# Performance work log

Hardware: AMD Instinct MI355X
Metric: run time of the kernel (lower is better)

Reference implementation:

```python
import jax, jax.numpy as jnp
import numpy as np

N_NODES = 100000
N_EDGES = 1600000
IN_DIM, HID_DIM, OUT_DIM = 128, 256, 128


def setup_inputs() -> dict:
    key = jax.random.key(0)
    ks = jax.random.split(key, 5)
    x = jax.random.normal(ks[0], (N_NODES, IN_DIM), dtype=jnp.float32)
    src = jax.random.randint(ks[1], (N_EDGES,), 0, N_NODES, dtype=jnp.int64)
    dst = jax.random.randint(ks[2], (N_EDGES,), 0, N_NODES, dtype=jnp.int64)
    # Glorot-ish init for linear weights (DGL GraphConv default), zero bias
    W1 = jax.random.normal(ks[3], (IN_DIM, HID_DIM), dtype=jnp.float32) * (1.0 / np.sqrt(IN_DIM))
    W2 = jax.random.normal(ks[4], (HID_DIM, OUT_DIM), dtype=jnp.float32) * (1.0 / np.sqrt(HID_DIM))
    b1 = jnp.zeros((HID_DIM,), dtype=jnp.float32)
    b2 = jnp.zeros((OUT_DIM,), dtype=jnp.float32)
    return {"x": x, "src": src, "dst": dst, "W1": W1, "b1": b1, "W2": W2, "b2": b2}


def _degree_norms(src, dst, n_nodes):
    # norm='both': D_out(src)^{-1/2} on messages, D_in(dst)^{-1/2} on aggregate;
    # degrees clamped to min 1 as in DGL.
    ones = jnp.ones(src.shape[0], dtype=jnp.float32)
    deg_out = jax.ops.segment_sum(ones, src, num_segments=n_nodes)
    deg_in = jax.ops.segment_sum(ones, dst, num_segments=n_nodes)
    norm_src = jax.lax.rsqrt(jnp.maximum(deg_out, 1.0))
    norm_dst = jax.lax.rsqrt(jnp.maximum(deg_in, 1.0))
    return norm_src, norm_dst


def _graph_conv(x, src, dst, W, b, norm_src, norm_dst):
    h = x * norm_src[:, None]                                  # [N, d]
    agg = jax.ops.segment_sum(h[src], dst, num_segments=x.shape[0])  # [N, d]
    agg = agg * norm_dst[:, None]
    return agg @ W + b


def reference(x, src, dst, W1, b1, W2, b2):
    norm_src, norm_dst = _degree_norms(src, dst, x.shape[0])
    h = jax.nn.relu(_graph_conv(x, src, dst, W1, b1, norm_src, norm_dst))
    out = _graph_conv(h, src, dst, W2, b2, norm_src, norm_dst)
    return out
```

## Files before the change

kernel.cpp:

```cpp
#include <hip/hip_runtime.h>

constexpr int N_NODES = 100000;
constexpr int N_EDGES = 1600000;
constexpr int DIN = 128, DHID = 256, DOUT = 128;

constexpr int NB = 256;
constexpr int BR = 391;
constexpr int CAP = 8192;
constexpr int NBLK1 = 512;
constexpr int CHUNK = (N_EDGES + NBLK1 - 1) / NBLK1;

typedef __bf16 bf16x8 __attribute__((ext_vector_type(8)));
typedef float f32x4 __attribute__((ext_vector_type(4)));

static __device__ __forceinline__ ushort f2bf(float f) {
    uint u = __float_as_uint(f);
    uint r = (u + 0x7FFFu + ((u >> 16) & 1u)) >> 16;
    return (ushort)r;
}
static __device__ __forceinline__ float bf2f(ushort h) {
    return __uint_as_float(((uint)h) << 16);
}
static __device__ __forceinline__ float bflo(uint w) { return __uint_as_float(w << 16); }
static __device__ __forceinline__ float bfhi(uint w) { return __uint_as_float(w & 0xFFFF0000u); }

__global__ __launch_bounds__(256) void part_kernel(const int* __restrict__ src,
                                                   const int* __restrict__ dst,
                                                   int* __restrict__ curA, int* __restrict__ curB,
                                                   uint2* __restrict__ ppair,
                                                   int* __restrict__ psv, int e) {
    __shared__ int hA[NB], hB[NB], rA[NB], rB[NB], cA[NB], cB[NB];
    const int t = threadIdx.x;
    const int b0 = blockIdx.x * CHUNK;
    const int cnt = min(e - b0, CHUNK);
    hA[t] = 0; hB[t] = 0; cA[t] = 0; cB[t] = 0;
    __syncthreads();
    for (int i = t; i < cnt; i += 256) {
        int s = src[b0 + i], d = dst[b0 + i];
        atomicAdd(&hA[d / BR], 1);
        atomicAdd(&hB[s / BR], 1);
    }
    __syncthreads();
    rA[t] = atomicAdd(&curA[t], hA[t]);
    rB[t] = atomicAdd(&curB[t], hB[t]);
    __syncthreads();
    for (int i = t; i < cnt; i += 256) {
        int s = src[b0 + i], d = dst[b0 + i];
        int bd = d / BR;
        int bs = s / BR;
        int p = rA[bd] + atomicAdd(&cA[bd], 1);
        if (p < CAP) ppair[(size_t)bd * CAP + p] = make_uint2((uint)d, (uint)s);
        int q = rB[bs] + atomicAdd(&cB[bs], 1);
        if (q < CAP) psv[(size_t)bs * CAP + q] = s;
    }
}

__global__ __launch_bounds__(512) void csrn_kernel(const int* __restrict__ curA,
                                                   const int* __restrict__ curB,
                                                   const uint2* __restrict__ ppair,
                                                   const int* __restrict__ psv,
                                                   int* __restrict__ csr,
                                                   int* __restrict__ rowstart,
                                                   float* __restrict__ ndst,
                                                   float* __restrict__ nsrc, int n, int e) {
    __shared__ ushort dloc[CAP];
    __shared__ uint sloc[CAP];
    __shared__ int hist[512], sc[512], exc[512], cur[512];
    __shared__ int sbst;
    const int t = threadIdx.x;
    const int b = blockIdx.x;
    const int first = b * BR;
    const int nr = min(BR, n - first);
    const int cntA = min(curA[b], CAP);
    const size_t base = (size_t)b * CAP;

    if (t < 256) sc[t] = curA[t];
    __syncthreads();
    for (int off = 1; off < 256; off <<= 1) {
        int add = 0;
        if (t < 256 && t >= off) add = sc[t - off];
        __syncthreads();
        if (t < 256) sc[t] += add;
        __syncthreads();
    }
    if (t == 0) {
        sbst = (b == 0) ? 0 : sc[b - 1];
        if (b == 0) rowstart[n] = e;
    }
    hist[t] = 0;
    cur[t] = 0;
    __syncthreads();
    const int bst = sbst;

    for (int i = t; i < cntA; i += 512) {
        uint2 ed = ppair[base + i];
        int dl = (int)ed.x - first;
        dloc[i] = (ushort)dl;
        sloc[i] = ed.y;
        atomicAdd(&hist[dl], 1);
    }
    __syncthreads();
    int h = hist[t];
    sc[t] = h;
    __syncthreads();
    for (int off = 1; off < 512; off <<= 1) {
        int add = (t >= off) ? sc[t - off] : 0;
        __syncthreads();
        sc[t] += add;
        __syncthreads();
    }
    exc[t] = sc[t] - h;
    if (t < nr) {
        rowstart[first + t] = bst + exc[t];
        ndst[first + t] = rsqrtf(fmaxf((float)h, 1.0f));
    }
    __syncthreads();
    for (int i = t; i < cntA; i += 512) {
        int dl = dloc[i];
        int p = exc[dl] + atomicAdd(&cur[dl], 1);
        csr[bst + p] = (int)sloc[i];
    }

    __syncthreads();
    hist[t] = 0;
    __syncthreads();
    const int cntB = min(curB[b], CAP);
    for (int i = t; i < cntB; i += 512) atomicAdd(&hist[psv[base + i] - first], 1);
    __syncthreads();
    if (t < nr) nsrc[first + t] = rsqrtf(fmaxf((float)hist[t], 1.0f));
}

__global__ __launch_bounds__(256) void prep_kernel(const float* __restrict__ x,
                                                   const float* __restrict__ nsrc,
                                                   ushort* __restrict__ xb,
                                                   const float* __restrict__ W1,
                                                   ushort* __restrict__ Wt1,
                                                   const float* __restrict__ W2,
                                                   ushort* __restrict__ Wt2, int n) {
    const int nxb = (n * 32 + 255) / 256;
    int blk = blockIdx.x;
    if (blk < nxb) {
        int i = blk * 256 + threadIdx.x;
        if (i < n * 32) {
            int row = i >> 5;
            float s = nsrc[row];
            float4 v = *(const float4*)&x[(size_t)i * 4];
            ushort4 o = {f2bf(v.x * s), f2bf(v.y * s), f2bf(v.z * s), f2bf(v.w * s)};
            *(ushort4*)&xb[(size_t)i * 4] = o;
        }
    } else if (blk < nxb + DIN * DHID / 256) {
        int i = (blk - nxb) * 256 + threadIdx.x;
        int k = i / DHID, c = i - k * DHID;
        Wt1[(size_t)c * DIN + k] = f2bf(W1[i]);
    } else {
        int i = (blk - nxb - DIN * DHID / 256) * 256 + threadIdx.x;
        int k = i / DOUT, c = i - k * DOUT;
        Wt2[(size_t)c * DHID + k] = f2bf(W2[i]);
    }
}

template <bool OUTBF16, bool ADDBIAS>
__global__ __launch_bounds__(256) void aggb_kernel(const ushort* __restrict__ Xb,
                                                   const int* __restrict__ csr,
                                                   const int* __restrict__ rowstart,
                                                   const float* __restrict__ ndst,
                                                   const float* __restrict__ bias,
                                                   float* __restrict__ outf,
                                                   ushort* __restrict__ outb, int n) {
    int g = threadIdx.x >> 4;
    int lane = threadIdx.x & 15;
    int d = blockIdx.x * 16 + g;
    if (d >= n) return;
    int beg = rowstart[d], end = rowstart[d + 1];
    const int fo = lane * 8;
    const ushort* Xp = Xb + fo;
    float acc[8];
#pragma unroll
    for (int j = 0; j < 8; j++) acc[j] = 0.f;

#define ACC8(v)                                 \
    do {                                        \
        acc[0] += bflo(v.x); acc[1] += bfhi(v.x); \
        acc[2] += bflo(v.y); acc[3] += bfhi(v.y); \
        acc[4] += bflo(v.z); acc[5] += bfhi(v.z); \
        acc[6] += bflo(v.w); acc[7] += bfhi(v.w); \
    } while (0)

    int k = beg;
    for (; k + 4 <= end; k += 4) {
        int s0 = csr[k], s1 = csr[k + 1], s2 = csr[k + 2], s3 = csr[k + 3];
        uint4 v0 = *(const uint4*)(Xp + (size_t)s0 * 128);
        uint4 v1 = *(const uint4*)(Xp + (size_t)s1 * 128);
        uint4 v2 = *(const uint4*)(Xp + (size_t)s2 * 128);
        uint4 v3 = *(const uint4*)(Xp + (size_t)s3 * 128);
        ACC8(v0);
        ACC8(v1);
        ACC8(v2);
        ACC8(v3);
    }
    for (; k < end; ++k) {
        uint4 v = *(const uint4*)(Xp + (size_t)csr[k] * 128);
        ACC8(v);
    }
#undef ACC8

    float nd = ndst[d];
#pragma unroll
    for (int j = 0; j < 8; j++) acc[j] *= nd;
    if constexpr (ADDBIAS) {
        float4 b0 = *(const float4*)&bias[fo];
        float4 b1 = *(const float4*)&bias[fo + 4];
        acc[0] += b0.x; acc[1] += b0.y; acc[2] += b0.z; acc[3] += b0.w;
        acc[4] += b1.x; acc[5] += b1.y; acc[6] += b1.z; acc[7] += b1.w;
    }
    if constexpr (OUTBF16) {
        uint4 o;
        o.x = (uint)f2bf(acc[0]) | ((uint)f2bf(acc[1]) << 16);
        o.y = (uint)f2bf(acc[2]) | ((uint)f2bf(acc[3]) << 16);
        o.z = (uint)f2bf(acc[4]) | ((uint)f2bf(acc[5]) << 16);
        o.w = (uint)f2bf(acc[6]) | ((uint)f2bf(acc[7]) << 16);
        *(uint4*)(outb + (size_t)d * 128 + fo) = o;
    } else {
        float4 o0 = {acc[0], acc[1], acc[2], acc[3]};
        float4 o1 = {acc[4], acc[5], acc[6], acc[7]};
        *(float4*)(outf + (size_t)d * 128 + fo) = o0;
        *(float4*)(outf + (size_t)d * 128 + fo + 4) = o1;
    }
}

__global__ __launch_bounds__(256) void fused64_kernel(const ushort* __restrict__ A,
                                                      const ushort* __restrict__ Wt1,
                                                      const float* __restrict__ b1,
                                                      const float* __restrict__ nsrc,
                                                      const ushort* __restrict__ Wt2,
                                                      ushort* __restrict__ T, int M) {
    __shared__ ushort Sa[64][128];
    __shared__ ushort H1[64][128];
    const int row0 = blockIdx.x * 64;
    const int t = threadIdx.x;
    const int w = t >> 6, lane = t & 63;
    const int l16 = lane & 15, lk = lane >> 4;

#pragma unroll
    for (int i = 0; i < 4; i++) {
        int idx = i * 256 + t;
        int r = idx >> 4, oct = idx & 15;
        int gr = row0 + r;
        uint4 v = make_uint4(0u, 0u, 0u, 0u);
        if (gr < M) v = *(const uint4*)&A[(size_t)gr * 128 + oct * 8];
        *(uint4*)((char*)&Sa[0][0] + r * 256 + (oct ^ (r & 15)) * 16) = v;
    }
    __syncthreads();

    f32x4 acc2[4][2];
#pragma unroll
    for (int i = 0; i < 4; i++)
#pragma unroll
        for (int j = 0; j < 2; j++) acc2[i][j] = (f32x4){0.f, 0.f, 0.f, 0.f};

    for (int kh = 0; kh < 2; kh++) {
        f32x4 acc1[2][4];
#pragma unroll
        for (int i = 0; i < 2; i++)
#pragma unroll
            for (int j = 0; j < 4; j++) acc1[i][j] = (f32x4){0.f, 0.f, 0.f, 0.f};

        bf16x8 af[2][4];
#pragma unroll
        for (int i = 0; i < 2; i++)
#pragma unroll
            for (int kb = 0; kb < 4; kb++) {
                int c = w * 32 + i * 16 + l16;
                af[i][kb] =
                    *(const bf16x8*)&Wt1[(size_t)(kh * 128 + c) * 128 + kb * 32 + lk * 8];
            }
#pragma unroll
        for (int kb = 0; kb < 4; kb++) {
            bf16x8 bf_[4];
#pragma unroll
            for (int j = 0; j < 4; j++) {
                int m = j * 16 + l16;
                bf_[j] = *(const bf16x8*)((const char*)&Sa[0][0] + m * 256 +
                                          ((kb * 4 + lk) ^ l16) * 16);
            }
#pragma unroll
            for (int i = 0; i < 2; i++)
#pragma unroll
                for (int j = 0; j < 4; j++)
                    acc1[i][j] =
                        __builtin_amdgcn_mfma_f32_16x16x32_bf16(af[i][kb], bf_[j], acc1[i][j], 0, 0, 0);
        }
        __syncthreads();

#pragma unroll
        for (int i = 0; i < 2; i++) {
            int cb = w * 32 + i * 16 + lk * 4;
            float4 bv = *(const float4*)&b1[kh * 128 + cb];
#pragma unroll
            for (int j = 0; j < 4; j++) {
                int m = j * 16 + l16;
                int gm = row0 + m;
                float ns = nsrc[gm < M ? gm : (M - 1)];
                ushort4 pk;
                pk.x = f2bf(fmaxf(acc1[i][j][0] + bv.x, 0.f) * ns);
                pk.y = f2bf(fmaxf(acc1[i][j][1] + bv.y, 0.f) * ns);
                pk.z = f2bf(fmaxf(acc1[i][j][2] + bv.z, 0.f) * ns);
                pk.w = f2bf(fmaxf(acc1[i][j][3] + bv.w, 0.f) * ns);
                int oct = cb >> 3;
                *(ushort4*)((char*)&H1[0][0] + m * 256 + ((oct ^ l16) & 15) * 16 +
                            (cb & 7) * 2) = pk;
            }
        }
        __syncthreads();

        bf16x8 wb[2][4];
#pragma unroll
        for (int j2 = 0; j2 < 2; j2++)
#pragma unroll
            for (int kb2 = 0; kb2 < 4; kb2++) {
                int c2 = w * 32 + j2 * 16 + l16;
                wb[j2][kb2] =
                    *(const bf16x8*)&Wt2[(size_t)c2 * 256 + kh * 128 + kb2 * 32 + lk * 8];
            }
#pragma unroll
        for (int kb2 = 0; kb2 < 4; kb2++) {
            bf16x8 ha[4];
#pragma unroll
            for (int i2 = 0; i2 < 4; i2++) {
                int m = i2 * 16 + l16;
                ha[i2] = *(const bf16x8*)((const char*)&H1[0][0] + m * 256 +
                                          ((kb2 * 4 + lk) ^ l16) * 16);
            }
#pragma unroll
            for (int i2 = 0; i2 < 4; i2++)
#pragma unroll
                for (int j2 = 0; j2 < 2; j2++)
                    acc2[i2][j2] = __builtin_amdgcn_mfma_f32_16x16x32_bf16(ha[i2], wb[j2][kb2],
                                                                           acc2[i2][j2], 0, 0, 0);
        }
    }

#pragma unroll
    for (int i2 = 0; i2 < 4; i2++) {
#pragma unroll
        for (int j2 = 0; j2 < 2; j2++) {
#pragma unroll
            for (int q = 0; q < 4; q++) {
                int r = row0 + i2 * 16 + lk * 4 + q;
                int c = w * 32 + j2 * 16 + l16;
                if (r < M) T[(size_t)r * DOUT + c] = f2bf(acc2[i2][j2][q]);
            }
        }
    }
}

extern "C" void kernel_launch(void* const* d_in, const int* in_sizes, int n_in,
                              void* d_out, int out_size, void* d_ws, size_t ws_size,
                              hipStream_t stream) {
    const float* x  = (const float*)d_in[0];
    const int*   src = (const int*)d_in[1];
    const int*   dst = (const int*)d_in[2];
    const float* W1 = (const float*)d_in[3];
    const float* b1 = (const float*)d_in[4];
    const float* W2 = (const float*)d_in[5];
    const float* b2 = (const float*)d_in[6];
    float* out = (float*)d_out;

    const int N = N_NODES, E = N_EDGES;

    size_t off = 0;
    auto carve = [&](size_t bytes) -> void* {
        void* p = (char*)d_ws + off;
        off += (bytes + 255) & ~(size_t)255;
        return p;
    };
    int* curA     = (int*)carve(NB * 4);
    int* curB     = (int*)carve(NB * 4);
    int* rowstart = (int*)carve((size_t)(N + 1) * 4);
    float* ndst   = (float*)carve((size_t)N * 4);
    float* nsrc   = (float*)carve((size_t)N * 4);
    int* csr      = (int*)carve((size_t)E * 4);
    ushort* Wt1   = (ushort*)carve(DIN * DHID * 2);
    ushort* Wt2   = (ushort*)carve(DHID * DOUT * 2);
    ushort* xb    = (ushort*)carve((size_t)N * DIN * 2);
    ushort* agg1b = (ushort*)carve((size_t)N * DIN * 2);
    ushort* tb    = (ushort*)carve((size_t)N * DOUT * 2);
    uint2* ppair  = (uint2*)carve((size_t)NB * CAP * 8);
    int*   psv    = (int*)carve((size_t)NB * CAP * 4);

    hipMemsetAsync(curA, 0, 2 * NB * 4, stream);

    part_kernel<<<NBLK1, 256, 0, stream>>>(src, dst, curA, curB, ppair, psv, E);
    csrn_kernel<<<NB, 512, 0, stream>>>(curA, curB, ppair, psv, csr, rowstart, ndst, nsrc, N, E);

    const int nxb = (N * 32 + 255) / 256;
    prep_kernel<<<nxb + DIN * DHID / 256 + DHID * DOUT / 256, 256, 0, stream>>>(
        x, nsrc, xb, W1, Wt1, W2, Wt2, N);

    aggb_kernel<true, false><<<(N + 15) / 16, 256, 0, stream>>>(xb, csr, rowstart, ndst, nullptr,
                                                                nullptr, agg1b, N);

    fused64_kernel<<<(N + 63) / 64, 256, 0, stream>>>(agg1b, Wt1, b1, nsrc, Wt2, tb, N);

    aggb_kernel<false, true><<<(N + 15) / 16, 256, 0, stream>>>(tb, csr, rowstart, ndst, b2,
                                                                out, nullptr, N);
}
```

Measured before the change: 240.1 us.

## Split gather aggregation into feature halves and fold prep work into partition kernels

```diff
diff --git a/kernel.cpp b/kernel.cpp
--- a/kernel.cpp
+++ b/kernel.cpp
@@ -28,15 +28,33 @@
                                                    const int* __restrict__ dst,
                                                    int* __restrict__ curA, int* __restrict__ curB,
                                                    uint2* __restrict__ ppair,
-                                                   int* __restrict__ psv, int e) {
+                                                   int* __restrict__ psv, int e,
+                                                   const float* __restrict__ W1,
+                                                   ushort* __restrict__ Wt1,
+                                                   const float* __restrict__ W2,
+                                                   ushort* __restrict__ Wt2) {
+    const int t = threadIdx.x;
+    if (blockIdx.x >= NBLK1) {
+        int i = (blockIdx.x - NBLK1) * 256 + t;
+        if (i < DIN * DHID) {
+            int k = i / DHID, c = i - k * DHID;
+            Wt1[(size_t)c * DIN + k] = f2bf(W1[i]);
+        } else {
+            i -= DIN * DHID;
+            int k = i / DOUT, c = i - k * DOUT;
+            Wt2[(size_t)c * DHID + k] = f2bf(W2[i]);
+        }
+        return;
+    }
+    __shared__ uint2 estage[CHUNK];
     __shared__ int hA[NB], hB[NB], rA[NB], rB[NB], cA[NB], cB[NB];
-    const int t = threadIdx.x;
     const int b0 = blockIdx.x * CHUNK;
     const int cnt = min(e - b0, CHUNK);
     hA[t] = 0; hB[t] = 0; cA[t] = 0; cB[t] = 0;
     __syncthreads();
     for (int i = t; i < cnt; i += 256) {
         int s = src[b0 + i], d = dst[b0 + i];
+        estage[i] = make_uint2((uint)d, (uint)s);
         atomicAdd(&hA[d / BR], 1);
         atomicAdd(&hB[s / BR], 1);
     }
@@ -45,13 +63,13 @@
     rB[t] = atomicAdd(&curB[t], hB[t]);
     __syncthreads();
     for (int i = t; i < cnt; i += 256) {
-        int s = src[b0 + i], d = dst[b0 + i];
-        int bd = d / BR;
-        int bs = s / BR;
+        uint2 ed = estage[i];
+        int bd = (int)ed.x / BR;
+        int bs = (int)ed.y / BR;
         int p = rA[bd] + atomicAdd(&cA[bd], 1);
-        if (p < CAP) ppair[(size_t)bd * CAP + p] = make_uint2((uint)d, (uint)s);
+        if (p < CAP) ppair[(size_t)bd * CAP + p] = ed;
         int q = rB[bs] + atomicAdd(&cB[bs], 1);
-        if (q < CAP) psv[(size_t)bs * CAP + q] = s;
+        if (q < CAP) psv[(size_t)bs * CAP + q] = (int)ed.y;
     }
 }
 
@@ -62,7 +80,9 @@
                                                    int* __restrict__ csr,
                                                    int* __restrict__ rowstart,
                                                    float* __restrict__ ndst,
-                                                   float* __restrict__ nsrc, int n, int e) {
+                                                   float* __restrict__ nsrc,
+                                                   const float* __restrict__ x,
+                                                   ushort* __restrict__ xb, int n, int e) {
     __shared__ ushort dloc[CAP];
     __shared__ uint sloc[CAP];
     __shared__ int hist[512], sc[512], exc[512], cur[512];
@@ -127,59 +147,45 @@
     const int cntB = min(curB[b], CAP);
     for (int i = t; i < cntB; i += 512) atomicAdd(&hist[psv[base + i] - first], 1);
     __syncthreads();
-    if (t < nr) nsrc[first + t] = rsqrtf(fmaxf((float)hist[t], 1.0f));
-}
-
-__global__ __launch_bounds__(256) void prep_kernel(const float* __restrict__ x,
-                                                   const float* __restrict__ nsrc,
-                                                   ushort* __restrict__ xb,
-                                                   const float* __restrict__ W1,
-                                                   ushort* __restrict__ Wt1,
-                                                   const float* __restrict__ W2,
-                                                   ushort* __restrict__ Wt2, int n) {
-    const int nxb = (n * 32 + 255) / 256;
-    int blk = blockIdx.x;
-    if (blk < nxb) {
-        int i = blk * 256 + threadIdx.x;
-        if (i < n * 32) {
-            int row = i >> 5;
-            float s = nsrc[row];
-            float4 v = *(const float4*)&x[(size_t)i * 4];
-            ushort4 o = {f2bf(v.x * s), f2bf(v.y * s), f2bf(v.z * s), f2bf(v.w * s)};
-            *(ushort4*)&xb[(size_t)i * 4] = o;
-        }
-    } else if (blk < nxb + DIN * DHID / 256) {
-        int i = (blk - nxb) * 256 + threadIdx.x;
-        int k = i / DHID, c = i - k * DHID;
-        Wt1[(size_t)c * DIN + k] = f2bf(W1[i]);
-    } else {
-        int i = (blk - nxb - DIN * DHID / 256) * 256 + threadIdx.x;
-        int k = i / DOUT, c = i - k * DOUT;
-        Wt2[(size_t)c * DHID + k] = f2bf(W2[i]);
+    float* nsv = (float*)exc;
+    if (t < nr) {
+        float v = rsqrtf(fmaxf((float)hist[t], 1.0f));
+        nsrc[first + t] = v;
+        nsv[t] = v;
+    }
+    __syncthreads();
+
+    const int rl = t >> 5, q = t & 31;
+    for (int i = rl; i < nr; i += 16) {
+        float s = nsv[i];
+        const size_t ro = (size_t)(first + i) * 128;
+        float4 v = *(const float4*)&x[ro + q * 4];
+        ushort4 o = {f2bf(v.x * s), f2bf(v.y * s), f2bf(v.z * s), f2bf(v.w * s)};
+        *(ushort4*)&xb[ro + q * 4] = o;
     }
 }
 
 template <bool OUTBF16, bool ADDBIAS>
-__global__ __launch_bounds__(256) void aggb_kernel(const ushort* __restrict__ Xb,
+__global__ __launch_bounds__(256) void aggh_kernel(const ushort* __restrict__ Xb,
                                                    const int* __restrict__ csr,
                                                    const int* __restrict__ rowstart,
                                                    const float* __restrict__ ndst,
                                                    const float* __restrict__ bias,
                                                    float* __restrict__ outf,
-                                                   ushort* __restrict__ outb, int n) {
-    int g = threadIdx.x >> 4;
-    int lane = threadIdx.x & 15;
-    int d = blockIdx.x * 16 + g;
+                                                   ushort* __restrict__ outb, int n, int half) {
+    int g = threadIdx.x >> 3;
+    int lane = threadIdx.x & 7;
+    int d = blockIdx.x * 32 + g;
     if (d >= n) return;
     int beg = rowstart[d], end = rowstart[d + 1];
-    const int fo = lane * 8;
+    const int fo = half * 64 + lane * 8;
     const ushort* Xp = Xb + fo;
     float acc[8];
 #pragma unroll
     for (int j = 0; j < 8; j++) acc[j] = 0.f;
 
-#define ACC8(v)                                 \
-    do {                                        \
+#define ACC8(v)                                   \
+    do {                                          \
         acc[0] += bflo(v.x); acc[1] += bfhi(v.x); \
         acc[2] += bflo(v.y); acc[3] += bfhi(v.y); \
         acc[4] += bflo(v.z); acc[5] += bfhi(v.z); \
@@ -390,18 +396,21 @@
 
     hipMemsetAsync(curA, 0, 2 * NB * 4, stream);
 
-    part_kernel<<<NBLK1, 256, 0, stream>>>(src, dst, curA, curB, ppair, psv, E);
-    csrn_kernel<<<NB, 512, 0, stream>>>(curA, curB, ppair, psv, csr, rowstart, ndst, nsrc, N, E);
-
-    const int nxb = (N * 32 + 255) / 256;
-    prep_kernel<<<nxb + DIN * DHID / 256 + DHID * DOUT / 256, 256, 0, stream>>>(
-        x, nsrc, xb, W1, Wt1, W2, Wt2, N);
-
-    aggb_kernel<true, false><<<(N + 15) / 16, 256, 0, stream>>>(xb, csr, rowstart, ndst, nullptr,
-                                                                nullptr, agg1b, N);
+    part_kernel<<<NBLK1 + 256, 256, 0, stream>>>(src, dst, curA, curB, ppair, psv, E,
+                                                 W1, Wt1, W2, Wt2);
+    csrn_kernel<<<NB, 512, 0, stream>>>(curA, curB, ppair, psv, csr, rowstart, ndst, nsrc,
+                                        x, xb, N, E);
+
+    const int gagg = (N + 31) / 32;
+    aggh_kernel<true, false><<<gagg, 256, 0, stream>>>(xb, csr, rowstart, ndst, nullptr,
+                                                       nullptr, agg1b, N, 0);
+    aggh_kernel<true, false><<<gagg, 256, 0, stream>>>(xb, csr, rowstart, ndst, nullptr,
+                                                       nullptr, agg1b, N, 1);
 
     fused64_kernel<<<(N + 63) / 64, 256, 0, stream>>>(agg1b, Wt1, b1, nsrc, Wt2, tb, N);
 
-    aggb_kernel<false, true><<<(N + 15) / 16, 256, 0, stream>>>(tb, csr, rowstart, ndst, b2,
-                                                                out, nullptr, N);
-}
+    aggh_kernel<false, true><<<gagg, 256, 0, stream>>>(tb, csr, rowstart, ndst, b2,
+                                                       out, nullptr, N, 0);
+    aggh_kernel<false, true><<<gagg, 256, 0, stream>>>(tb, csr, rowstart, ndst, b2,
+                                                       out, nullptr, N, 1);
+}
```

Result: faster. 233.5 us (-2.8%).
